# Kernel optimization log

Measured on AMD Instinct MI355X. Metric: run time of the kernel, lower is better.

The kernel has to match this reference:

```python
import jax, jax.numpy as jnp
import numpy as np

B, F, H, W = 1, 6, 20, 26
S = F * H * W            # 3120 tokens
DIM, NH, HD = 1536, 12, 128
C = HD // 2              # 64 rotary channels
T_C = C - 2 * (C // 3)   # 22 temporal channels
H_C = C // 3             # 21
W_C = C // 3             # 21
LOCAL_FRAMES = 4         # local_attn_size (in frames)
SINK_FRAMES = 1          # sink_size (in frames)
EPS = 1e-6
MAX_POS = 1024


def _angle_table(n_ch):
    inv = 1.0 / (10000.0 ** (np.arange(n_ch, dtype=np.float64) / n_ch))
    return np.outer(np.arange(MAX_POS, dtype=np.float64), inv)


def setup_inputs() -> dict:
    key = jax.random.key(0)
    ks = jax.random.split(key, 8)
    sc = 0.02
    ang = np.concatenate([_angle_table(T_C), _angle_table(H_C), _angle_table(W_C)], axis=1)  # [1024, 64]
    return {
        "x": jax.random.normal(ks[0], (B, S, DIM), jnp.float32),
        "seq_lens": jnp.array([S], jnp.int32),
        "grid_sizes": jnp.array([[F, H, W]], jnp.int32),
        "freqs_cos": jnp.asarray(np.cos(ang), jnp.float32),
        "freqs_sin": jnp.asarray(np.sin(ang), jnp.float32),
        "Wq": jax.random.normal(ks[1], (DIM, DIM), jnp.float32) * sc,
        "bq": jnp.zeros((DIM,), jnp.float32),
        "Wk": jax.random.normal(ks[2], (DIM, DIM), jnp.float32) * sc,
        "bk": jnp.zeros((DIM,), jnp.float32),
        "Wv": jax.random.normal(ks[3], (DIM, DIM), jnp.float32) * sc,
        "bv": jnp.zeros((DIM,), jnp.float32),
        "Wo": jax.random.normal(ks[4], (DIM, DIM), jnp.float32) * sc,
        "bo": jnp.zeros((DIM,), jnp.float32),
        "gq": jnp.ones((DIM,), jnp.float32),
        "gk": jnp.ones((DIM,), jnp.float32),
    }


def _rms_norm(x, g):
    # WanRMSNorm: x * rsqrt(mean(x^2) + eps) * weight
    return x * jax.lax.rsqrt(jnp.mean(x * x, axis=-1, keepdims=True) + EPS) * g


def _rope_apply(x, freqs_cos, freqs_sin):
    # x: [B, S, NH, HD]; per-token 3D (f,h,w) rotary on consecutive pairs.
    pos = jnp.arange(S)
    f = pos // (H * W)
    hh = (pos // W) % H
    ww = pos % W
    cos_t, cos_h, cos_w = freqs_cos[:, :T_C], freqs_cos[:, T_C:T_C + H_C], freqs_cos[:, T_C + H_C:]
    sin_t, sin_h, sin_w = freqs_sin[:, :T_C], freqs_sin[:, T_C:T_C + H_C], freqs_sin[:, T_C + H_C:]
    cos = jnp.concatenate([cos_t[f], cos_h[hh], cos_w[ww]], axis=-1)[None, :, None, :]  # [1,S,1,C]
    sin = jnp.concatenate([sin_t[f], sin_h[hh], sin_w[ww]], axis=-1)[None, :, None, :]
    xp = x.reshape(B, S, NH, C, 2)
    xr, xi = xp[..., 0], xp[..., 1]
    out = jnp.stack([xr * cos - xi * sin, xr * sin + xi * cos], axis=-1)
    return out.reshape(B, S, NH, HD)


def _block_mask():
    # frame-causal + local window (in frames) + sink frames: [S, S] bool
    fid = jnp.arange(S) // (H * W)
    fi, fj = fid[:, None], fid[None, :]
    return (fj <= fi) & ((fi - fj < LOCAL_FRAMES) | (fj < SINK_FRAMES))


def reference(x, seq_lens, grid_sizes, freqs_cos, freqs_sin,
              Wq, bq, Wk, bk, Wv, bv, Wo, bo, gq, gk):
    q = _rms_norm(x @ Wq + bq, gq).reshape(B, S, NH, HD)
    k = _rms_norm(x @ Wk + bk, gk).reshape(B, S, NH, HD)
    v = (x @ Wv + bv).reshape(B, S, NH, HD)
    rq = _rope_apply(q, freqs_cos, freqs_sin)
    rk = _rope_apply(k, freqs_cos, freqs_sin)
    scale = 1.0 / jnp.sqrt(jnp.asarray(HD, x.dtype))
    scores = jnp.einsum('bind,bjnd->bnij', rq, rk) * scale  # [B,NH,S,S]
    scores = jnp.where(_block_mask()[None, None], scores, jnp.finfo(scores.dtype).min)
    attn = jax.nn.softmax(scores, axis=-1)
    out = jnp.einsum('bnij,bjnd->bind', attn, v).reshape(B, S, DIM)
    return out @ Wo + bo
```

## Files before the change

kernel.cpp:

```cpp
#include <hip/hip_runtime.h>
#include <hip/hip_bf16.h>
#include <stdint.h>

typedef short v8s __attribute__((ext_vector_type(8)));
typedef float v4f __attribute__((ext_vector_type(4)));
typedef unsigned short u16;

#define S_LEN 3120
#define DIMN 1536
#define NHEAD 12
#define HDIM 128
#define FRM 520
#define NT128 25
#define TASKS_PH 86
#define TOTAL_TASKS 1032
#define SCALE_QK 0.088388347648318447f
#define MAXOFF 12.0f

__device__ __forceinline__ v4f mfma16(v8s a, v8s b, v4f c) {
  return __builtin_amdgcn_mfma_f32_16x16x32_bf16(a, b, c, 0, 0, 0);
}
__device__ __forceinline__ float b2f(u16 u) {
  union { float f; unsigned int i; } x; x.i = ((unsigned int)u) << 16; return x.f;
}
__device__ __forceinline__ u16 f2b(float f) {
  union { float f; unsigned int i; } x; x.f = f;
  unsigned int r = x.i + 0x7FFFu + ((x.i >> 16) & 1u);
  return (u16)(r >> 16);
}
__device__ __forceinline__ void async16(const void* g, void* l) {
  __builtin_amdgcn_global_load_lds(
      (__attribute__((address_space(1))) const void*)g,
      (__attribute__((address_space(3))) void*)l, 16, 0, 0);
}

__global__ void detect_dtype(const u16* __restrict__ w, int* __restrict__ flag) {
  __shared__ int sh;
  int t = threadIdx.x;
  if (t == 0) sh = 0;
  __syncthreads();
  u16 m0 = (u16)(w[2 * t] & 0x7FFF);
  u16 m1 = (u16)(w[2 * t + 1] & 0x7FFF);
  if (m0 >= 0x4480 || m1 >= 0x4480) atomicOr(&sh, 1);
  __syncthreads();
  if (t == 0) *flag = sh;
}

struct ConvArgs { const void* src[9]; u16* dst[9]; int n[9]; };
__global__ __launch_bounds__(256) void convert_all(ConvArgs a, const int* __restrict__ flag) {
  int id = blockIdx.y;
  int n = a.n[id];
  int isf = *flag;
  const float* sf = (const float*)a.src[id];
  const u16* sb = (const u16*)a.src[id];
  u16* d = a.dst[id];
  for (int i = blockIdx.x * 256 + threadIdx.x; i < n; i += gridDim.x * 256)
    d[i] = isf ? f2b(sf[i]) : sb[i];
}

struct TPArgs { const void* in[4]; u16* out[4]; };
__global__ __launch_bounds__(256) void transpose_conv4(TPArgs a, const int* __restrict__ flag) {
  __shared__ u16 tile[32][33];
  int z = blockIdx.z;
  const float* inf = (const float*)a.in[z];
  const u16* inb = (const u16*)a.in[z];
  u16* out = a.out[z];
  int isf = *flag;
  int t = threadIdx.x, tx = t & 31, ty = t >> 5;
  int gr0 = blockIdx.y * 32, gc0 = blockIdx.x * 32;
#pragma unroll
  for (int i = 0; i < 4; ++i) {
    int r = ty + i * 8;
    size_t idx = (size_t)(gr0 + r) * DIMN + gc0 + tx;
    tile[r][tx] = isf ? f2b(inf[idx]) : inb[idx];
  }
  __syncthreads();
#pragma unroll
  for (int i = 0; i < 4; ++i) {
    int r = ty + i * 8;
    out[(size_t)(gc0 + r) * DIMN + gr0 + tx] = tile[tx][r];
  }
}

__global__ __launch_bounds__(256) void transpose16(const u16* __restrict__ in,
                                                   u16* __restrict__ out,
                                                   int rows, int cols) {
  __shared__ u16 tile[32][33];
  int t = threadIdx.x;
  int tx = t & 31, ty = t >> 5;
  int gr0 = blockIdx.y * 32, gc0 = blockIdx.x * 32;
#pragma unroll
  for (int i = 0; i < 4; ++i) {
    int r = ty + i * 8;
    int gr = gr0 + r, gc = gc0 + tx;
    if (gr < rows && gc < cols) tile[r][tx] = in[(size_t)gr * cols + gc];
  }
  __syncthreads();
#pragma unroll
  for (int i = 0; i < 4; ++i) {
    int r = ty + i * 8;
    int orow = gc0 + r, ocol = gr0 + tx;
    if (orow < cols && ocol < rows) out[(size_t)orow * rows + ocol] = tile[tx][r];
  }
}

__global__ __launch_bounds__(256) void gemm3(
    const u16* __restrict__ A,
    const u16* BT0, const u16* BT1, const u16* BT2,
    const u16* b0, const u16* b1, const u16* b2,
    void* C0, void* C1, void* C2, int M, const int* __restrict__ flag, int dyn) {
  const u16* BT; const u16* bias; void* C;
  if (blockIdx.z == 0)      { BT = BT0; bias = b0; C = C0; }
  else if (blockIdx.z == 1) { BT = BT1; bias = b1; C = C1; }
  else                      { BT = BT2; bias = b2; C = C2; }
  int f32out = dyn ? *flag : 0;
  __shared__ __align__(16) short As[128 * 64];
  __shared__ __align__(16) short Bs[128 * 64];
  int t = threadIdx.x, w = t >> 6, l = t & 63;
  int ln = l & 15, lg = l >> 4;
  int m0 = blockIdx.y * 128, n0 = blockIdx.x * 128;
  int lr = l >> 3;
  int gl = (l & 7) ^ lr;
  const u16* gAp[4]; const u16* gBp[4];
  short* lAp[4]; short* lBp[4];
#pragma unroll
  for (int i = 0; i < 4; ++i) {
    int c = w * 4 + i;
    int arow = min(m0 + c * 8 + lr, M - 1);
    gAp[i] = A + (size_t)arow * DIMN + gl * 8;
    lAp[i] = As + c * 512;
    int brow = n0 + c * 8 + lr;
    gBp[i] = BT + (size_t)brow * DIMN + gl * 8;
    lBp[i] = Bs + c * 512;
  }
  int wm = w & 1, wn = w >> 1;
  int aoff[2][4], boff[2][4];
#pragma unroll
  for (int ks = 0; ks < 2; ++ks)
#pragma unroll
    for (int i = 0; i < 4; ++i) {
      int ar = wm * 64 + i * 16 + ln;
      int br = wn * 64 + i * 16 + ln;
      aoff[ks][i] = ar * 64 + (((ks * 4 + lg) ^ (ar & 7)) * 8);
      boff[ks][i] = br * 64 + (((ks * 4 + lg) ^ (br & 7)) * 8);
    }
  v4f acc[4][4] = {};
  for (int k0 = 0; k0 < DIMN; k0 += 64) {
    __syncthreads();
#pragma unroll
    for (int i = 0; i < 4; ++i) {
      async16(gAp[i] + k0, lAp[i]);
      async16(gBp[i] + k0, lBp[i]);
    }
    __syncthreads();
#pragma unroll
    for (int ks = 0; ks < 2; ++ks) {
      v8s af[4], bfr[4];
#pragma unroll
      for (int i = 0; i < 4; ++i) af[i] = *(const v8s*)(As + aoff[ks][i]);
#pragma unroll
      for (int i = 0; i < 4; ++i) bfr[i] = *(const v8s*)(Bs + boff[ks][i]);
#pragma unroll
      for (int i = 0; i < 4; ++i)
#pragma unroll
        for (int j = 0; j < 4; ++j) acc[i][j] = mfma16(af[i], bfr[j], acc[i][j]);
    }
  }
#pragma unroll
  for (int i = 0; i < 4; ++i) {
    int rb = m0 + wm * 64 + i * 16 + lg * 4;
#pragma unroll
    for (int j = 0; j < 4; ++j) {
      int col = n0 + wn * 64 + j * 16 + ln;
      float bv = b2f(bias[col]);
#pragma unroll
      for (int r = 0; r < 4; ++r) {
        int grow = rb + r;
        if (grow < M) {
          size_t idx = (size_t)grow * DIMN + col;
          float val = acc[i][j][r] + bv;
          if (f32out) ((float*)C)[idx] = val;
          else        ((u16*)C)[idx] = f2b(val);
        }
      }
    }
  }
}

__global__ __launch_bounds__(256) void norm_rope(u16* __restrict__ Q, u16* __restrict__ K,
                                                 const u16* __restrict__ gq,
                                                 const u16* __restrict__ gk,
                                                 const u16* __restrict__ fcos,
                                                 const u16* __restrict__ fsin) {
  int s = blockIdx.x;
  u16* base = (blockIdx.y == 0 ? Q : K) + (size_t)s * DIMN;
  const u16* g = (blockIdx.y == 0) ? gq : gk;
  int t = threadIdx.x;
  int e = t * 6;
  float x[6];
#pragma unroll
  for (int i = 0; i < 6; ++i) x[i] = b2f(base[e + i]);
  float ss = 0.f;
#pragma unroll
  for (int i = 0; i < 6; ++i) ss += x[i] * x[i];
#pragma unroll
  for (int off = 32; off > 0; off >>= 1) ss += __shfl_xor(ss, off);
  __shared__ float red[4];
  if ((t & 63) == 0) red[t >> 6] = ss;
  __syncthreads();
  float tot = red[0] + red[1] + red[2] + red[3];
  float rs = rsqrtf(tot * (1.0f / DIMN) + 1e-6f);
  int f = s / FRM;
  int hh = (s / 26) % 20;
  int ww = s % 26;
#pragma unroll
  for (int u = 0; u < 3; ++u) {
    int e0 = e + 2 * u;
    int c = (e0 & 127) >> 1;
    int p = (c < 22) ? f : ((c < 43) ? hh : ww);
    float co = b2f(fcos[p * 64 + c]);
    float si = b2f(fsin[p * 64 + c]);
    float xr = x[2 * u] * rs * b2f(g[e0]);
    float xi = x[2 * u + 1] * rs * b2f(g[e0 + 1]);
    base[e0]     = f2b(xr * co - xi * si);
    base[e0 + 1] = f2b(xr * si + xi * co);
  }
}

__global__ __launch_bounds__(256) void attn_block(const u16* __restrict__ Q,
                                                  const u16* __restrict__ K,
                                                  const u16* __restrict__ VT,
                                                  u16* __restrict__ Po,
                                                  float* __restrict__ Pl) {
  __shared__ __align__(16) short Ks[64 * 128];
  __shared__ __align__(16) short Vs[128 * 64];
  __shared__ __align__(16) short Pt[4][32 * 72];
  int t = threadIdx.x, w = t >> 6, l = t & 63;
  int ln = l & 15, lg = l >> 4;
  int task = blockIdx.x;
  int head = task / TASKS_PH, tid = task % TASKS_PH;
  int tile = 0, frame = 0;
  {
    int acc = 0;
    for (tile = 0; tile < NT128; ++tile) {
      int q0t = tile * 128;
      int f_lo = q0t / FRM;
      int f_hi = min(q0t + 127, S_LEN - 1) / FRM;
      int fstart = max(0, f_lo - 3);
      int sink = fstart > 0;
      int nf = f_hi - fstart + 1 + sink;
      if (tid < acc + nf) {
        int c = tid - acc;
        frame = sink ? (c == 0 ? 0 : fstart + c - 1) : (fstart + c);
        break;
      }
      acc += nf;
    }
  }
  int q0 = tile * 128 + w * 32;
  v8s qf[2][4];
  bool rowok[2][4];
#pragma unroll
  for (int g = 0; g < 2; ++g) {
    int row = min(q0 + g * 16 + ln, S_LEN - 1);
    const u16* qp = Q + (size_t)row * DIMN + head * HDIM + lg * 8;
#pragma unroll
    for (int c = 0; c < 4; ++c) qf[g][c] = *(const v8s*)(qp + c * 32);
#pragma unroll
    for (int r = 0; r < 4; ++r) {
      int qr = q0 + g * 16 + lg * 4 + r;
      int fi = (qr < S_LEN) ? qr / FRM : -1;
      rowok[g][r] = (frame <= fi) && ((fi - frame) < 4 || frame == 0);
    }
  }
  float lsum[2][4] = {};
  v4f o[2][8] = {};
  int kbeg = frame * FRM, kend = kbeg + FRM;
  for (int kb = kbeg; kb < kend; kb += 64) {
    __syncthreads();
#pragma unroll
    for (int i = 0; i < 4; ++i) {
      int c = w * 4 + i;
      int n = c * 64 + l;
      int r = n >> 4;
      int gl = (n & 15) ^ (r & 15);
      int krow = min(kb + r, S_LEN - 1);
      async16((const char*)K + (size_t)krow * (DIMN * 2) + head * 256 + gl * 16,
              (char*)Ks + c * 1024);
    }
#pragma unroll
    for (int i = 0; i < 4; ++i) {
      int c = w * 4 + i;
      int n = c * 64 + l;
      int d = n >> 3;
      int gl = (n & 7) ^ (d & 7);
      async16((const char*)VT + (size_t)(head * HDIM + d) * (S_LEN * 2) + (size_t)kb * 2 + gl * 16,
              (char*)Vs + c * 1024);
    }
    __syncthreads();
    v4f s[2][4] = {};
#pragma unroll
    for (int kg = 0; kg < 4; ++kg) {
      int kr = kg * 16 + ln;
#pragma unroll
      for (int c = 0; c < 4; ++c) {
        v8s kf = *(const v8s*)(Ks + kr * 128 + (((c * 4 + lg) ^ ln) * 8));
        s[0][kg] = mfma16(qf[0][c], kf, s[0][kg]);
        s[1][kg] = mfma16(qf[1][c], kf, s[1][kg]);
      }
    }
#pragma unroll
    for (int g = 0; g < 2; ++g)
#pragma unroll
      for (int kg = 0; kg < 4; ++kg) {
        bool jv = (kb + kg * 16 + ln) < kend;
#pragma unroll
        for (int r = 0; r < 4; ++r) {
          float p = (rowok[g][r] && jv) ? __expf(s[g][kg][r] * SCALE_QK - MAXOFF) : 0.f;
          lsum[g][r] += p;
          Pt[w][(g * 16 + lg * 4 + r) * 72 + kg * 16 + ln] = f2b(p);
        }
      }
#pragma unroll
    for (int kc = 0; kc < 2; ++kc) {
      v8s pf0 = *(const v8s*)(&Pt[w][ln * 72 + kc * 32 + lg * 8]);
      v8s pf1 = *(const v8s*)(&Pt[w][(16 + ln) * 72 + kc * 32 + lg * 8]);
#pragma unroll
      for (int d = 0; d < 8; ++d) {
        int rr = d * 16 + ln;
        v8s vf = *(const v8s*)(Vs + rr * 64 + (((kc * 4 + lg) ^ (ln & 7)) * 8));
        o[0][d] = mfma16(pf0, vf, o[0][d]);
        o[1][d] = mfma16(pf1, vf, o[1][d]);
      }
    }
  }
#pragma unroll
  for (int g = 0; g < 2; ++g)
#pragma unroll
    for (int r = 0; r < 4; ++r) {
      float v = lsum[g][r];
      v += __shfl_xor(v, 1);
      v += __shfl_xor(v, 2);
      v += __shfl_xor(v, 4);
      v += __shfl_xor(v, 8);
      lsum[g][r] = v;
    }
  size_t pbase = (size_t)task * (128 * 128);
#pragma unroll
  for (int g = 0; g < 2; ++g)
#pragma unroll
    for (int d = 0; d < 8; ++d)
#pragma unroll
      for (int r = 0; r < 4; ++r) {
        int lrow = w * 32 + g * 16 + lg * 4 + r;
        Po[pbase + lrow * 128 + d * 16 + ln] = f2b(o[g][d][r]);
      }
  if (ln == 0) {
#pragma unroll
    for (int g = 0; g < 2; ++g)
#pragma unroll
      for (int r = 0; r < 4; ++r)
        Pl[task * 128 + w * 32 + g * 16 + lg * 4 + r] = lsum[g][r];
  }
}

__global__ __launch_bounds__(256) void attn_combine(const u16* __restrict__ Po,
                                                    const float* __restrict__ Pl,
                                                    u16* __restrict__ Oa) {
  int tile = blockIdx.x, h = blockIdx.y;
  int accv = 0, nf = 0;
  for (int q = 0; q < NT128; ++q) {
    int q0t = q * 128;
    int f_lo = q0t / FRM;
    int f_hi = min(q0t + 127, S_LEN - 1) / FRM;
    int fstart = max(0, f_lo - 3);
    int sink = fstart > 0;
    nf = f_hi - fstart + 1 + sink;
    if (q == tile) break;
    accv += nf;
  }
  int base = h * TASKS_PH + accv;
  int t = threadIdx.x;
  int row = t >> 1, seg = (t & 1) * 64;
  int grow = tile * 128 + row;
  if (grow >= S_LEN) return;
  float lsum = 0.f;
  float ao[64];
#pragma unroll
  for (int j = 0; j < 64; ++j) ao[j] = 0.f;
  for (int c = 0; c < nf; ++c) {
    int task = base + c;
    lsum += Pl[task * 128 + row];
    const u16* p = Po + (size_t)task * 16384 + row * 128 + seg;
#pragma unroll
    for (int v = 0; v < 8; ++v) {
      v8s x = *(const v8s*)(p + v * 8);
#pragma unroll
      for (int j = 0; j < 8; ++j) ao[v * 8 + j] += b2f((u16)x[j]);
    }
  }
  float inv = 1.0f / lsum;
  u16* dst = Oa + (size_t)grow * DIMN + h * HDIM + seg;
#pragma unroll
  for (int v = 0; v < 8; ++v) {
    v8s res;
#pragma unroll
    for (int j = 0; j < 8; ++j) res[j] = (short)f2b(ao[v * 8 + j] * inv);
    *(v8s*)(dst + v * 8) = res;
  }
}

extern "C" void kernel_launch(void* const* d_in, const int* in_sizes, int n_in,
                              void* d_out, int out_size, void* d_ws, size_t ws_size,
                              hipStream_t stream) {
  (void)n_in; (void)out_size; (void)ws_size;
  int* flag = (int*)d_ws;
  u16* ws = (u16*)d_ws;
  size_t off = 16;
  const size_t SD = (size_t)S_LEN * DIMN;
  const size_t WW = (size_t)DIMN * DIMN;
  const size_t NPO = (size_t)TOTAL_TASKS * 128 * 128;
  auto alloc = [&](size_t n) { u16* p = ws + off; off += (n + 7) & ~(size_t)7; return p; };
  u16* Xc  = alloc(SD);
  u16* Fc  = alloc(65536);
  u16* Fs  = alloc(65536);
  u16* bqc = alloc(1536); u16* bkc = alloc(1536); u16* bvc = alloc(1536); u16* boc = alloc(1536);
  u16* gqc = alloc(1536); u16* gkc = alloc(1536);
  u16* Qr = alloc(SD); u16* Kr = alloc(SD); u16* Vr = alloc(SD); u16* Oa = alloc(SD);
  u16* WoT = alloc(WW);
  u16* WqT = alloc(WW); u16* WkT = alloc(WW); u16* WvT = alloc(WW);
  alloc(NPO - 3 * WW);
  float* Pl = (float*)alloc((size_t)TOTAL_TASKS * 128 * 2);
  u16* Po = WqT;
  u16* VT = Xc;

  detect_dtype<<<1, 256, 0, stream>>>((const u16*)d_in[5], flag);

  ConvArgs ca;
  const int srcIdx[9] = {0, 3, 4, 6, 8, 10, 12, 13, 14};
  u16* dsts[9] = {Xc, Fc, Fs, bqc, bkc, bvc, boc, gqc, gkc};
  for (int i = 0; i < 9; ++i) {
    ca.src[i] = d_in[srcIdx[i]];
    ca.dst[i] = dsts[i];
    ca.n[i] = in_sizes[srcIdx[i]];
  }
  convert_all<<<dim3(512, 9), 256, 0, stream>>>(ca, flag);

  TPArgs tp;
  tp.in[0] = d_in[5];  tp.out[0] = WqT;
  tp.in[1] = d_in[7];  tp.out[1] = WkT;
  tp.in[2] = d_in[9];  tp.out[2] = WvT;
  tp.in[3] = d_in[11]; tp.out[3] = WoT;
  dim3 b256(256);
  transpose_conv4<<<dim3(48, 48, 4), b256, 0, stream>>>(tp, flag);
  gemm3<<<dim3(12, 25, 3), b256, 0, stream>>>(Xc, WqT, WkT, WvT, bqc, bkc, bvc,
                                              Qr, Kr, Vr, S_LEN, flag, 0);
  norm_rope<<<dim3(S_LEN, 2), b256, 0, stream>>>(Qr, Kr, gqc, gkc, Fc, Fs);
  transpose16<<<dim3(48, 98), b256, 0, stream>>>(Vr, VT, S_LEN, DIMN);
  attn_block<<<dim3(TOTAL_TASKS), b256, 0, stream>>>(Qr, Kr, VT, Po, Pl);
  attn_combine<<<dim3(NT128, NHEAD), b256, 0, stream>>>(Po, Pl, Oa);
  gemm3<<<dim3(12, 25, 1), b256, 0, stream>>>(Oa, WoT, WoT, WoT, boc, boc, boc,
                                              d_out, d_out, d_out, S_LEN, flag, 1);
}
```

Before: 396.2 us.

## Merge prep kernels, inline dtype probe, shrink attention key tile to 32

Removes the separate dtype-detect kernel by having each kernel probe the weight bits inline, and fuses the conversion and transpose launches into one prep kernel. The attention kernel now walks keys in 32-row steps with smaller LDS tiles and precomputed, incrementing load pointers. Row clamping is dropped in favour of padded workspace buffers. The aim is fewer launches and higher attention occupancy, at the cost of each thread redundantly reading 256 probe values and twice as many barriers per key range.

```diff
diff --git a/kernel.cpp b/kernel.cpp
--- a/kernel.cpp
+++ b/kernel.cpp
@@ -14,6 +14,7 @@
 #define NT128 25
 #define TASKS_PH 86
 #define TOTAL_TASKS 1032
+#define NSTEP 17
 #define SCALE_QK 0.088388347648318447f
 #define MAXOFF 12.0f
 
@@ -33,52 +34,50 @@
       (__attribute__((address_space(1))) const void*)g,
       (__attribute__((address_space(3))) void*)l, 16, 0, 0);
 }
-
-__global__ void detect_dtype(const u16* __restrict__ w, int* __restrict__ flag) {
-  __shared__ int sh;
+__device__ __forceinline__ int probe_f32(const u16* __restrict__ w) {
+  int bad = 0;
+#pragma unroll
+  for (int i = 0; i < 256; ++i) bad |= (int)((u16)(w[i] & 0x7FFF) >= 0x4480);
+  return bad;
+}
+
+struct PrepArgs {
+  const void* tin[4]; u16* tout[4];
+  const void* csrc[9]; u16* cdst[9]; int cn[9];
+};
+__global__ __launch_bounds__(256) void prep(PrepArgs a, const u16* __restrict__ probe) {
+  int isf = probe_f32(probe);
+  int z = blockIdx.z;
   int t = threadIdx.x;
-  if (t == 0) sh = 0;
-  __syncthreads();
-  u16 m0 = (u16)(w[2 * t] & 0x7FFF);
-  u16 m1 = (u16)(w[2 * t + 1] & 0x7FFF);
-  if (m0 >= 0x4480 || m1 >= 0x4480) atomicOr(&sh, 1);
-  __syncthreads();
-  if (t == 0) *flag = sh;
-}
-
-struct ConvArgs { const void* src[9]; u16* dst[9]; int n[9]; };
-__global__ __launch_bounds__(256) void convert_all(ConvArgs a, const int* __restrict__ flag) {
-  int id = blockIdx.y;
-  int n = a.n[id];
-  int isf = *flag;
-  const float* sf = (const float*)a.src[id];
-  const u16* sb = (const u16*)a.src[id];
-  u16* d = a.dst[id];
-  for (int i = blockIdx.x * 256 + threadIdx.x; i < n; i += gridDim.x * 256)
-    d[i] = isf ? f2b(sf[i]) : sb[i];
-}
-
-struct TPArgs { const void* in[4]; u16* out[4]; };
-__global__ __launch_bounds__(256) void transpose_conv4(TPArgs a, const int* __restrict__ flag) {
-  __shared__ u16 tile[32][33];
-  int z = blockIdx.z;
-  const float* inf = (const float*)a.in[z];
-  const u16* inb = (const u16*)a.in[z];
-  u16* out = a.out[z];
-  int isf = *flag;
-  int t = threadIdx.x, tx = t & 31, ty = t >> 5;
-  int gr0 = blockIdx.y * 32, gc0 = blockIdx.x * 32;
-#pragma unroll
-  for (int i = 0; i < 4; ++i) {
-    int r = ty + i * 8;
-    size_t idx = (size_t)(gr0 + r) * DIMN + gc0 + tx;
-    tile[r][tx] = isf ? f2b(inf[idx]) : inb[idx];
-  }
-  __syncthreads();
-#pragma unroll
-  for (int i = 0; i < 4; ++i) {
-    int r = ty + i * 8;
-    out[(size_t)(gc0 + r) * DIMN + gr0 + tx] = tile[tx][r];
+  if (z < 4) {
+    __shared__ u16 tile[32][33];
+    const float* inf = (const float*)a.tin[z];
+    const u16* inb = (const u16*)a.tin[z];
+    u16* out = a.tout[z];
+    int tx = t & 31, ty = t >> 5;
+    int gr0 = blockIdx.y * 32, gc0 = blockIdx.x * 32;
+#pragma unroll
+    for (int i = 0; i < 4; ++i) {
+      int r = ty + i * 8;
+      size_t idx = (size_t)(gr0 + r) * DIMN + gc0 + tx;
+      tile[r][tx] = isf ? f2b(inf[idx]) : inb[idx];
+    }
+    __syncthreads();
+#pragma unroll
+    for (int i = 0; i < 4; ++i) {
+      int r = ty + i * 8;
+      out[(size_t)(gc0 + r) * DIMN + gr0 + tx] = tile[tx][r];
+    }
+  } else {
+    int id = z - 4;
+    int n = a.cn[id];
+    const float* sf = (const float*)a.csrc[id];
+    const u16* sb = (const u16*)a.csrc[id];
+    u16* d = a.cdst[id];
+    int bidx = blockIdx.y * gridDim.x + blockIdx.x;
+    int stride = gridDim.x * gridDim.y * 256;
+    for (int i = bidx * 256 + t; i < n; i += stride)
+      d[i] = isf ? f2b(sf[i]) : sb[i];
   }
 }
 
@@ -108,12 +107,13 @@
     const u16* __restrict__ A,
     const u16* BT0, const u16* BT1, const u16* BT2,
     const u16* b0, const u16* b1, const u16* b2,
-    void* C0, void* C1, void* C2, int M, const int* __restrict__ flag, int dyn) {
+    void* C0, void* C1, void* C2, int M,
+    const u16* __restrict__ probe, int dyn) {
   const u16* BT; const u16* bias; void* C;
   if (blockIdx.z == 0)      { BT = BT0; bias = b0; C = C0; }
   else if (blockIdx.z == 1) { BT = BT1; bias = b1; C = C1; }
   else                      { BT = BT2; bias = b2; C = C2; }
-  int f32out = dyn ? *flag : 0;
+  int f32out = dyn ? probe_f32(probe) : 0;
   __shared__ __align__(16) short As[128 * 64];
   __shared__ __align__(16) short Bs[128 * 64];
   int t = threadIdx.x, w = t >> 6, l = t & 63;
@@ -232,9 +232,9 @@
                                                   const u16* __restrict__ VT,
                                                   u16* __restrict__ Po,
                                                   float* __restrict__ Pl) {
-  __shared__ __align__(16) short Ks[64 * 128];
-  __shared__ __align__(16) short Vs[128 * 64];
-  __shared__ __align__(16) short Pt[4][32 * 72];
+  __shared__ __align__(16) short Ks[32 * 128];
+  __shared__ __align__(16) short Vs[128 * 32];
+  __shared__ __align__(16) short Pt[4][32 * 40];
   int t = threadIdx.x, w = t >> 6, l = t & 63;
   int ln = l & 15, lg = l >> 4;
   int task = blockIdx.x;
@@ -262,7 +262,7 @@
   bool rowok[2][4];
 #pragma unroll
   for (int g = 0; g < 2; ++g) {
-    int row = min(q0 + g * 16 + ln, S_LEN - 1);
+    int row = q0 + g * 16 + ln;
     const u16* qp = Q + (size_t)row * DIMN + head * HDIM + lg * 8;
 #pragma unroll
     for (int c = 0; c < 4; ++c) qf[g][c] = *(const v8s*)(qp + c * 32);
@@ -276,35 +276,34 @@
   float lsum[2][4] = {};
   v4f o[2][8] = {};
   int kbeg = frame * FRM, kend = kbeg + FRM;
-  for (int kb = kbeg; kb < kend; kb += 64) {
+  const u16* kp[2]; const u16* vp[2];
+  char* kd[2]; char* vd[2];
+#pragma unroll
+  for (int i = 0; i < 2; ++i) {
+    int n = w * 128 + i * 64 + l;
+    int kr = n >> 4, kgl = (n & 15) ^ (kr & 15);
+    kp[i] = K + (size_t)(kbeg + kr) * DIMN + head * HDIM + kgl * 8;
+    kd[i] = (char*)Ks + (size_t)(w * 2 + i) * 1024;
+    int vdim = n >> 2, vgl = (n & 3) ^ (vdim & 3);
+    vp[i] = VT + (size_t)(head * HDIM + vdim) * S_LEN + kbeg + vgl * 8;
+    vd[i] = (char*)Vs + (size_t)(w * 2 + i) * 1024;
+  }
+  for (int it = 0; it < NSTEP; ++it) {
+    int kb = kbeg + it * 32;
     __syncthreads();
 #pragma unroll
-    for (int i = 0; i < 4; ++i) {
-      int c = w * 4 + i;
-      int n = c * 64 + l;
-      int r = n >> 4;
-      int gl = (n & 15) ^ (r & 15);
-      int krow = min(kb + r, S_LEN - 1);
-      async16((const char*)K + (size_t)krow * (DIMN * 2) + head * 256 + gl * 16,
-              (char*)Ks + c * 1024);
-    }
-#pragma unroll
-    for (int i = 0; i < 4; ++i) {
-      int c = w * 4 + i;
-      int n = c * 64 + l;
-      int d = n >> 3;
-      int gl = (n & 7) ^ (d & 7);
-      async16((const char*)VT + (size_t)(head * HDIM + d) * (S_LEN * 2) + (size_t)kb * 2 + gl * 16,
-              (char*)Vs + c * 1024);
+    for (int i = 0; i < 2; ++i) {
+      async16(kp[i], kd[i]);
+      async16(vp[i], vd[i]);
     }
     __syncthreads();
-    v4f s[2][4] = {};
-#pragma unroll
-    for (int kg = 0; kg < 4; ++kg) {
+    v4f s[2][2] = {};
+#pragma unroll
+    for (int kg = 0; kg < 2; ++kg) {
       int kr = kg * 16 + ln;
 #pragma unroll
       for (int c = 0; c < 4; ++c) {
-        v8s kf = *(const v8s*)(Ks + kr * 128 + (((c * 4 + lg) ^ ln) * 8));
+        v8s kf = *(const v8s*)(&Ks[kr * 128 + (((c * 4 + lg) ^ (kr & 15)) * 8)]);
         s[0][kg] = mfma16(qf[0][c], kf, s[0][kg]);
         s[1][kg] = mfma16(qf[1][c], kf, s[1][kg]);
       }
@@ -312,27 +311,26 @@
 #pragma unroll
     for (int g = 0; g < 2; ++g)
 #pragma unroll
-      for (int kg = 0; kg < 4; ++kg) {
+      for (int kg = 0; kg < 2; ++kg) {
         bool jv = (kb + kg * 16 + ln) < kend;
 #pragma unroll
         for (int r = 0; r < 4; ++r) {
           float p = (rowok[g][r] && jv) ? __expf(s[g][kg][r] * SCALE_QK - MAXOFF) : 0.f;
           lsum[g][r] += p;
-          Pt[w][(g * 16 + lg * 4 + r) * 72 + kg * 16 + ln] = f2b(p);
+          Pt[w][(g * 16 + lg * 4 + r) * 40 + kg * 16 + ln] = f2b(p);
         }
       }
-#pragma unroll
-    for (int kc = 0; kc < 2; ++kc) {
-      v8s pf0 = *(const v8s*)(&Pt[w][ln * 72 + kc * 32 + lg * 8]);
-      v8s pf1 = *(const v8s*)(&Pt[w][(16 + ln) * 72 + kc * 32 + lg * 8]);
-#pragma unroll
-      for (int d = 0; d < 8; ++d) {
-        int rr = d * 16 + ln;
-        v8s vf = *(const v8s*)(Vs + rr * 64 + (((kc * 4 + lg) ^ (ln & 7)) * 8));
-        o[0][d] = mfma16(pf0, vf, o[0][d]);
-        o[1][d] = mfma16(pf1, vf, o[1][d]);
-      }
-    }
+    v8s pf0 = *(const v8s*)(&Pt[w][ln * 40 + lg * 8]);
+    v8s pf1 = *(const v8s*)(&Pt[w][(16 + ln) * 40 + lg * 8]);
+#pragma unroll
+    for (int d = 0; d < 8; ++d) {
+      int rr = d * 16 + ln;
+      v8s vf = *(const v8s*)(&Vs[rr * 32 + ((lg ^ (rr & 3)) * 8)]);
+      o[0][d] = mfma16(pf0, vf, o[0][d]);
+      o[1][d] = mfma16(pf1, vf, o[1][d]);
+    }
+#pragma unroll
+    for (int i = 0; i < 2; ++i) { kp[i] += 32 * DIMN; vp[i] += 32; }
   }
 #pragma unroll
   for (int g = 0; g < 2; ++g)
@@ -414,51 +412,48 @@
                               void* d_out, int out_size, void* d_ws, size_t ws_size,
                               hipStream_t stream) {
   (void)n_in; (void)out_size; (void)ws_size;
-  int* flag = (int*)d_ws;
   u16* ws = (u16*)d_ws;
   size_t off = 16;
   const size_t SD = (size_t)S_LEN * DIMN;
   const size_t WW = (size_t)DIMN * DIMN;
   const size_t NPO = (size_t)TOTAL_TASKS * 128 * 128;
   auto alloc = [&](size_t n) { u16* p = ws + off; off += (n + 7) & ~(size_t)7; return p; };
-  u16* Xc  = alloc(SD);
+  u16* Xc  = alloc(SD + 256);
   u16* Fc  = alloc(65536);
   u16* Fs  = alloc(65536);
   u16* bqc = alloc(1536); u16* bkc = alloc(1536); u16* bvc = alloc(1536); u16* boc = alloc(1536);
   u16* gqc = alloc(1536); u16* gkc = alloc(1536);
-  u16* Qr = alloc(SD); u16* Kr = alloc(SD); u16* Vr = alloc(SD); u16* Oa = alloc(SD);
+  u16* Qr = alloc(SD + (size_t)128 * DIMN);
+  u16* Kr = alloc(SD + (size_t)64 * DIMN);
+  u16* Vr = alloc(SD); u16* Oa = alloc(SD);
   u16* WoT = alloc(WW);
   u16* WqT = alloc(WW); u16* WkT = alloc(WW); u16* WvT = alloc(WW);
   alloc(NPO - 3 * WW);
   float* Pl = (float*)alloc((size_t)TOTAL_TASKS * 128 * 2);
   u16* Po = WqT;
   u16* VT = Xc;
-
-  detect_dtype<<<1, 256, 0, stream>>>((const u16*)d_in[5], flag);
-
-  ConvArgs ca;
+  const u16* probe = (const u16*)d_in[5];
+
+  PrepArgs pa;
+  pa.tin[0] = d_in[5];  pa.tout[0] = WqT;
+  pa.tin[1] = d_in[7];  pa.tout[1] = WkT;
+  pa.tin[2] = d_in[9];  pa.tout[2] = WvT;
+  pa.tin[3] = d_in[11]; pa.tout[3] = WoT;
   const int srcIdx[9] = {0, 3, 4, 6, 8, 10, 12, 13, 14};
   u16* dsts[9] = {Xc, Fc, Fs, bqc, bkc, bvc, boc, gqc, gkc};
   for (int i = 0; i < 9; ++i) {
-    ca.src[i] = d_in[srcIdx[i]];
-    ca.dst[i] = dsts[i];
-    ca.n[i] = in_sizes[srcIdx[i]];
-  }
-  convert_all<<<dim3(512, 9), 256, 0, stream>>>(ca, flag);
-
-  TPArgs tp;
-  tp.in[0] = d_in[5];  tp.out[0] = WqT;
-  tp.in[1] = d_in[7];  tp.out[1] = WkT;
-  tp.in[2] = d_in[9];  tp.out[2] = WvT;
-  tp.in[3] = d_in[11]; tp.out[3] = WoT;
+    pa.csrc[i] = d_in[srcIdx[i]];
+    pa.cdst[i] = dsts[i];
+    pa.cn[i] = in_sizes[srcIdx[i]];
+  }
   dim3 b256(256);
-  transpose_conv4<<<dim3(48, 48, 4), b256, 0, stream>>>(tp, flag);
+  prep<<<dim3(48, 48, 13), b256, 0, stream>>>(pa, probe);
   gemm3<<<dim3(12, 25, 3), b256, 0, stream>>>(Xc, WqT, WkT, WvT, bqc, bkc, bvc,
-                                              Qr, Kr, Vr, S_LEN, flag, 0);
+                                              Qr, Kr, Vr, S_LEN, probe, 0);
   norm_rope<<<dim3(S_LEN, 2), b256, 0, stream>>>(Qr, Kr, gqc, gkc, Fc, Fs);
   transpose16<<<dim3(48, 98), b256, 0, stream>>>(Vr, VT, S_LEN, DIMN);
   attn_block<<<dim3(TOTAL_TASKS), b256, 0, stream>>>(Qr, Kr, VT, Po, Pl);
   attn_combine<<<dim3(NT128, NHEAD), b256, 0, stream>>>(Po, Pl, Oa);
   gemm3<<<dim3(12, 25, 1), b256, 0, stream>>>(Oa, WoT, WoT, WoT, boc, boc, boc,
-                                              d_out, d_out, d_out, S_LEN, flag, 1);
-}
+                                              d_out, d_out, d_out, S_LEN, probe, 1);
+}
```

After: 597.5 us. 1.51x slower.
